# Kernel optimization log

Hardware: AMD Instinct MI355X
Metric: run time of the kernel (lower is better)

## Reference

```python
import jax, jax.numpy as jnp
import numpy as np

H = 16
D_MODEL = 1024
D_K = D_MODEL // H
WINDOW = 50
ROPE_BASE = 10000.0


def _rope_tables(seq_len, dim, dtype):
    inv_freq = 1.0 / (ROPE_BASE ** (jnp.arange(0, dim, 2, dtype=jnp.float32) / dim))
    t = jnp.arange(seq_len, dtype=jnp.float32)
    freqs = t[:, None] * inv_freq[None, :]          # [S, dim/2]
    emb = jnp.concatenate([freqs, freqs], axis=-1)  # [S, dim]
    return jnp.cos(emb).astype(dtype), jnp.sin(emb).astype(dtype)


def _rotate_half(x):
    d = x.shape[-1] // 2
    return jnp.concatenate([-x[..., d:], x[..., :d]], axis=-1)


def setup_inputs() -> dict:
    key = jax.random.key(0)
    ks = jax.random.split(key, 11)
    B, S = 2, 2048
    scale = 1.0 / np.sqrt(D_MODEL)
    inp = {
        'query': jax.random.normal(ks[0], (B, S, D_MODEL), jnp.float32),
        'key':   jax.random.normal(ks[1], (B, S, D_MODEL), jnp.float32),
        'value': jax.random.normal(ks[2], (B, S, D_MODEL), jnp.float32),
        'Wq': jax.random.normal(ks[3], (D_MODEL, D_MODEL), jnp.float32) * scale,
        'bq': jnp.zeros((D_MODEL,), jnp.float32),
        'Wk': jax.random.normal(ks[4], (D_MODEL, D_MODEL), jnp.float32) * scale,
        'bk': jnp.zeros((D_MODEL,), jnp.float32),
        'Wv': jax.random.normal(ks[5], (D_MODEL, D_MODEL), jnp.float32) * scale,
        'bv': jnp.zeros((D_MODEL,), jnp.float32),
        'Wo': jax.random.normal(ks[6], (D_MODEL, D_MODEL), jnp.float32) * scale,
        'bo': jnp.zeros((D_MODEL,), jnp.float32),
    }
    return inp


def reference(query, key, value, Wq, bq, Wk, bk, Wv, bv, Wo, bo):
    B, S, _ = query.shape
    # QKV projections (torch Linear: x @ W.T + b), split into heads -> [B,H,S,Dk]
    def proj(x, W, b):
        return (x @ W.T + b).reshape(B, S, H, D_K).transpose(0, 2, 1, 3)
    q = proj(query, Wq, bq)
    k = proj(key, Wk, bk)
    v = proj(value, Wv, bv)

    cos, sin = _rope_tables(S, D_K, q.dtype)  # [S, Dk]
    q = q * cos + _rotate_half(q) * sin
    k = k * cos + _rotate_half(k) * sin

    scores = jnp.einsum('bhqd,bhkd->bhqk', q, k) / np.sqrt(D_K)
    # sliding-window mask: |i-j| <= WINDOW
    idx = jnp.arange(S)
    dist = jnp.abs(idx[None, :] - idx[:, None])  # [S, S]
    scores = jnp.where(dist <= WINDOW, scores, jnp.asarray(-1e9, scores.dtype))

    p = jax.nn.softmax(scores, axis=-1)
    out = jnp.einsum('bhqk,bhkd->bhqd', p, v)          # [B,H,S,Dk]
    out = out.transpose(0, 2, 1, 3).reshape(B, S, D_MODEL)
    return out @ Wo.T + bo
```

## Files before the change

kernel.cpp:

```cpp
#include <hip/hip_runtime.h>
#include <hip/hip_bf16.h>
#include <math.h>

typedef __bf16 bf16_t;
typedef __bf16 bf16x8 __attribute__((ext_vector_type(8)));
typedef float floatx4 __attribute__((ext_vector_type(4)));
typedef unsigned int u32;

#define NHEAD 16

__device__ __forceinline__ void gload_lds16(const void* g, void* l) {
    __builtin_amdgcn_global_load_lds((const __attribute__((address_space(1))) u32*)g,
                                     (__attribute__((address_space(3))) u32*)l, 16, 0, 0);
}

__global__ __launch_bounds__(256) void k_prep(
    const float* __restrict__ q, const float* __restrict__ k, const float* __restrict__ v,
    const float* __restrict__ wq, const float* __restrict__ wk,
    const float* __restrict__ wv, const float* __restrict__ wo,
    bf16_t* __restrict__ Xq, bf16_t* __restrict__ Xk, bf16_t* __restrict__ Xv,
    bf16_t* __restrict__ Wqb, bf16_t* __restrict__ Wkb, bf16_t* __restrict__ Wvb,
    bf16_t* __restrict__ Wob, float* __restrict__ ct, float* __restrict__ st)
{
    int b = blockIdx.x;
    if (b < 8192) {
        const float* src; bf16_t* dst; int off;
        if      (b < 2048) { src = q;  dst = Xq;  off = b; }
        else if (b < 4096) { src = k;  dst = Xk;  off = b - 2048; }
        else if (b < 6144) { src = v;  dst = Xv;  off = b - 4096; }
        else if (b < 6656) { src = wq; dst = Wqb; off = b - 6144; }
        else if (b < 7168) { src = wk; dst = Wkb; off = b - 6656; }
        else if (b < 7680) { src = wv; dst = Wvb; off = b - 7168; }
        else               { src = wo; dst = Wob; off = b - 7680; }
        int i = (off * 256 + threadIdx.x) * 8;
        float4 a = *(const float4*)(src + i);
        float4 c = *(const float4*)(src + i + 4);
        bf16x8 o;
        o[0]=(bf16_t)a.x; o[1]=(bf16_t)a.y; o[2]=(bf16_t)a.z; o[3]=(bf16_t)a.w;
        o[4]=(bf16_t)c.x; o[5]=(bf16_t)c.y; o[6]=(bf16_t)c.z; o[7]=(bf16_t)c.w;
        *(bf16x8*)(dst + i) = o;
    } else {
        int idx = (b - 8192) * 256 + threadIdx.x;
        int s = idx >> 5, i = idx & 31;
        float e = (float)(2 * i) / 64.0f;
        float invf = 1.0f / powf(10000.0f, e);
        float ang = (float)s * invf;
        ct[idx] = cosf(ang);
        st[idx] = sinf(ang);
    }
}

__global__ __launch_bounds__(256,2) void k_gemm_qkv(
    const bf16_t* __restrict__ Xq, const bf16_t* __restrict__ Xk, const bf16_t* __restrict__ Xv,
    const bf16_t* __restrict__ Wqb, const bf16_t* __restrict__ Wkb, const bf16_t* __restrict__ Wvb,
    const float* __restrict__ bq, const float* __restrict__ bk, const float* __restrict__ bv,
    bf16_t* __restrict__ Qr, bf16_t* __restrict__ Kr, bf16_t* __restrict__ Vh,
    const float* __restrict__ ct, const float* __restrict__ st)
{
    __shared__ bf16_t As[2][128*32];
    __shared__ bf16_t Bs[2][128*32];

    int b0 = blockIdx.x;
    int wg = (b0 & 7) * 96 + (b0 >> 3);
    int id  = wg >> 8;
    int bid = wg & 255;

    const bf16_t* A   = (id==0) ? Xq  : (id==1) ? Xk  : Xv;
    const bf16_t* Wt  = (id==0) ? Wqb : (id==1) ? Wkb : Wvb;
    const float*  bias= (id==0) ? bq  : (id==1) ? bk  : bv;
    bf16_t* out = (id==0) ? Qr : (id==1) ? Kr : Vh;
    bool do_rope = (id < 2);

    int bm = (bid >> 3) << 7;
    int bn = (bid & 7) << 7;
    int tid = threadIdx.x;
    int l = tid & 63, wid = tid >> 6;
    int wr = wid >> 1, wc = wid & 1;
    int lane16 = l & 15, hi8 = (l >> 4) << 3;

    floatx4 acc[4][4];
    #pragma unroll
    for (int i = 0; i < 4; ++i)
        #pragma unroll
        for (int j = 0; j < 4; ++j) acc[i][j] = (floatx4){0.f,0.f,0.f,0.f};

    int srow = tid >> 2, scol = (tid & 3) << 3;
    const bf16_t* Ab = A  + ((size_t)(bm + srow) << 10) + scol;
    const bf16_t* Bb = Wt + ((size_t)(bn + srow) << 10) + scol;

    #pragma unroll
    for (int i2 = 0; i2 < 2; ++i2) {
        gload_lds16(Ab + (i2 << 16), &As[0][(tid + (i2<<8)) << 3]);
        gload_lds16(Bb + (i2 << 16), &Bs[0][(tid + (i2<<8)) << 3]);
    }
    __syncthreads();

    int cur = 0;
    for (int t = 0; t < 32; ++t) {
        if (t < 31) {
            int k0 = (t + 1) << 5;
            #pragma unroll
            for (int i2 = 0; i2 < 2; ++i2) {
                gload_lds16(Ab + k0 + (i2 << 16), &As[cur^1][(tid + (i2<<8)) << 3]);
                gload_lds16(Bb + k0 + (i2 << 16), &Bs[cur^1][(tid + (i2<<8)) << 3]);
            }
        }
        bf16x8 af[4], bfr[4];
        #pragma unroll
        for (int i = 0; i < 4; ++i)
            af[i]  = *(const bf16x8*)&As[cur][((wr<<6) + (i<<4) + lane16)*32 + hi8];
        #pragma unroll
        for (int j = 0; j < 4; ++j)
            bfr[j] = *(const bf16x8*)&Bs[cur][((wc<<6) + (j<<4) + lane16)*32 + hi8];
        #pragma unroll
        for (int i = 0; i < 4; ++i)
            #pragma unroll
            for (int j = 0; j < 4; ++j)
                acc[i][j] = __builtin_amdgcn_mfma_f32_16x16x32_bf16(af[i], bfr[j], acc[i][j], 0, 0, 0);
        __syncthreads();
        cur ^= 1;
    }

    int h = (bn + (wc<<6)) >> 6;
    #pragma unroll
    for (int i = 0; i < 4; ++i) {
        #pragma unroll
        for (int r = 0; r < 4; ++r) {
            int m  = bm + (wr<<6) + (i<<4) + ((l>>4)<<2) + r;
            int b_ = m >> 11, s_ = m & 2047;
            size_t ob = ((((size_t)(b_*NHEAD + h)) << 11) + s_) << 6;
            if (do_rope) {
                #pragma unroll
                for (int j = 0; j < 2; ++j) {
                    int d = (j<<4) + lane16;
                    float lo = acc[i][j][r]   + bias[bn + (wc<<6) + d];
                    float hv = acc[i][j+2][r] + bias[bn + (wc<<6) + d + 32];
                    float c = ct[(s_<<5) + d], sn = st[(s_<<5) + d];
                    out[ob + d]      = (bf16_t)(lo*c - hv*sn);
                    out[ob + d + 32] = (bf16_t)(hv*c + lo*sn);
                }
            } else {
                #pragma unroll
                for (int j = 0; j < 4; ++j) {
                    int d = (j<<4) + lane16;
                    out[ob + d] = (bf16_t)(acc[i][j][r] + bias[bn + (wc<<6) + d]);
                }
            }
        }
    }
}

__global__ __launch_bounds__(256,2) void k_gemm_o(
    const bf16_t* __restrict__ A, const bf16_t* __restrict__ Wt,
    const float* __restrict__ bias, float* __restrict__ out)
{
    __shared__ bf16_t As[2][128*32];
    __shared__ bf16_t Bs[2][128*32];

    int b0 = blockIdx.x;
    int bid = (b0 & 7) * 32 + (b0 >> 3);
    int bm = (bid >> 3) << 7;
    int bn = (bid & 7) << 7;
    int tid = threadIdx.x;
    int l = tid & 63, wid = tid >> 6;
    int wr = wid >> 1, wc = wid & 1;
    int lane16 = l & 15, hi8 = (l >> 4) << 3;

    floatx4 acc[4][4];
    #pragma unroll
    for (int i = 0; i < 4; ++i)
        #pragma unroll
        for (int j = 0; j < 4; ++j) acc[i][j] = (floatx4){0.f,0.f,0.f,0.f};

    int srow = tid >> 2, scol = (tid & 3) << 3;
    const bf16_t* Ab = A  + ((size_t)(bm + srow) << 10) + scol;
    const bf16_t* Bb = Wt + ((size_t)(bn + srow) << 10) + scol;

    #pragma unroll
    for (int i2 = 0; i2 < 2; ++i2) {
        gload_lds16(Ab + (i2 << 16), &As[0][(tid + (i2<<8)) << 3]);
        gload_lds16(Bb + (i2 << 16), &Bs[0][(tid + (i2<<8)) << 3]);
    }
    __syncthreads();

    int cur = 0;
    for (int t = 0; t < 32; ++t) {
        if (t < 31) {
            int k0 = (t + 1) << 5;
            #pragma unroll
            for (int i2 = 0; i2 < 2; ++i2) {
                gload_lds16(Ab + k0 + (i2 << 16), &As[cur^1][(tid + (i2<<8)) << 3]);
                gload_lds16(Bb + k0 + (i2 << 16), &Bs[cur^1][(tid + (i2<<8)) << 3]);
            }
        }
        bf16x8 af[4], bfr[4];
        #pragma unroll
        for (int i = 0; i < 4; ++i)
            af[i]  = *(const bf16x8*)&As[cur][((wr<<6) + (i<<4) + lane16)*32 + hi8];
        #pragma unroll
        for (int j = 0; j < 4; ++j)
            bfr[j] = *(const bf16x8*)&Bs[cur][((wc<<6) + (j<<4) + lane16)*32 + hi8];
        #pragma unroll
        for (int i = 0; i < 4; ++i)
            #pragma unroll
            for (int j = 0; j < 4; ++j)
                acc[i][j] = __builtin_amdgcn_mfma_f32_16x16x32_bf16(af[i], bfr[j], acc[i][j], 0, 0, 0);
        __syncthreads();
        cur ^= 1;
    }

    #pragma unroll
    for (int i = 0; i < 4; ++i)
        #pragma unroll
        for (int r = 0; r < 4; ++r) {
            int m = bm + (wr<<6) + (i<<4) + ((l>>4)<<2) + r;
            #pragma unroll
            for (int j = 0; j < 4; ++j) {
                int n = bn + (wc<<6) + (j<<4) + lane16;
                out[((size_t)m << 10) + n] = acc[i][j][r] + bias[n];
            }
        }
}

__global__ __launch_bounds__(256,2) void k_attn(
    const bf16_t* __restrict__ Qr, const bf16_t* __restrict__ Kr,
    const bf16_t* __restrict__ Vh, bf16_t* __restrict__ AO)
{
    __shared__ char smem[51200];
    bf16_t* KsPs = (bf16_t*)smem;
    bf16_t* Vt   = (bf16_t*)(smem + 25600);

    int q0 = blockIdx.x << 6;
    int h = blockIdx.y, b_ = blockIdx.z;
    int kstart = q0 - 64; if (kstart < 0) kstart = 0;
    int kend   = q0 + 128; if (kend > 2048) kend = 2048;
    int NR = kend - kstart;

    int tid = threadIdx.x, l = tid & 63, w = tid >> 6;
    int lane16 = l & 15, hi8 = (l >> 4) << 3;

    const bf16_t* Kbase = Kr + (((((size_t)(b_*NHEAD + h)) << 11) + kstart) << 6);
    const bf16_t* Vbase = Vh + (((((size_t)(b_*NHEAD + h)) << 11) + kstart) << 6);

    #pragma unroll
    for (int it = 0; it < 6; ++it) {
        int c = tid + (it << 8);
        int y = c << 4;
        int row = y >> 7, oz = y & 127;
        int srw = row < NR ? row : NR - 1;
        int src = (srw << 7) + (oz ^ ((row & 7) << 4));
        gload_lds16((const char*)Kbase + src, (char*)KsPs + y);
    }
    #pragma unroll
    for (int it = 0; it < 6; ++it) {
        int c = tid + (it << 8);
        int jd = c >> 3, d0 = (c & 7) << 3;
        int js = jd < NR ? jd : NR - 1;
        bf16x8 v8 = *(const bf16x8*)(Vbase + (js << 6) + d0);
        #pragma unroll
        for (int t = 0; t < 8; ++t) Vt[(d0 + t) * 200 + jd] = v8[t];
    }
    int qs = q0 + (w << 4) + lane16;
    const bf16_t* Qbase = Qr + (((((size_t)(b_*NHEAD + h)) << 11) + qs) << 6);
    bf16x8 qf0 = *(const bf16x8*)(Qbase + hi8);
    bf16x8 qf1 = *(const bf16x8*)(Qbase + 32 + hi8);

    __syncthreads();

    floatx4 sc[12];
    #pragma unroll
    for (int kt = 0; kt < 12; ++kt) {
        int row = (kt << 4) + lane16;
        int base = (row << 7) + (hi8 << 1);
        int swz = (row & 7) << 4;
        bf16x8 kf0 = *(const bf16x8*)((const char*)KsPs + (base ^ swz));
        bf16x8 kf1 = *(const bf16x8*)((const char*)KsPs + ((base + 64) ^ swz));
        floatx4 a = (floatx4){0.f,0.f,0.f,0.f};
        a = __builtin_amdgcn_mfma_f32_16x16x32_bf16(qf0, kf0, a, 0, 0, 0);
        a = __builtin_amdgcn_mfma_f32_16x16x32_bf16(qf1, kf1, a, 0, 0, 0);
        sc[kt] = a;
    }

    float inv_[4];
    #pragma unroll
    for (int r = 0; r < 4; ++r) {
        int qrow = q0 + (w << 4) + ((l >> 4) << 2) + r;
        float mx = -1e30f;
        #pragma unroll
        for (int kt = 0; kt < 12; ++kt) {
            int ks = kstart + (kt << 4) + lane16;
            int dd = qrow - ks; dd = dd < 0 ? -dd : dd;
            float sv = sc[kt][r] * 0.125f;
            sv = (dd <= 50 && ks < kend) ? sv : -1e30f;
            sc[kt][r] = sv;
            mx = fmaxf(mx, sv);
        }
        #pragma unroll
        for (int off = 1; off < 16; off <<= 1) mx = fmaxf(mx, __shfl_xor(mx, off));
        float sum = 0.f;
        #pragma unroll
        for (int kt = 0; kt < 12; ++kt) {
            float p = __expf(sc[kt][r] - mx);
            sc[kt][r] = p;
            sum += p;
        }
        #pragma unroll
        for (int off = 1; off < 16; off <<= 1) sum += __shfl_xor(sum, off);
        inv_[r] = 1.0f / sum;
    }

    __syncthreads();

    bf16_t* Pw = KsPs + w * 16 * 200;
    #pragma unroll
    for (int r = 0; r < 4; ++r) {
        int prow = ((l >> 4) << 2) + r;
        #pragma unroll
        for (int kt = 0; kt < 12; ++kt)
            Pw[prow * 200 + (kt << 4) + lane16] = (bf16_t)(sc[kt][r] * inv_[r]);
    }

    floatx4 oc[4];
    #pragma unroll
    for (int dt = 0; dt < 4; ++dt) oc[dt] = (floatx4){0.f,0.f,0.f,0.f};
    #pragma unroll
    for (int ks = 0; ks < 6; ++ks) {
        bf16x8 pf = *(const bf16x8*)&Pw[lane16 * 200 + (ks << 5) + hi8];
        #pragma unroll
        for (int dt = 0; dt < 4; ++dt) {
            bf16x8 vf = *(const bf16x8*)&Vt[((dt << 4) + lane16) * 200 + (ks << 5) + hi8];
            oc[dt] = __builtin_amdgcn_mfma_f32_16x16x32_bf16(pf, vf, oc[dt], 0, 0, 0);
        }
    }
    #pragma unroll
    for (int dt = 0; dt < 4; ++dt)
        #pragma unroll
        for (int r = 0; r < 4; ++r) {
            int qq = q0 + (w << 4) + ((l >> 4) << 2) + r;
            AO[(((size_t)(b_ * 2048 + qq)) << 10) + (h << 6) + (dt << 4) + lane16] = (bf16_t)oc[dt][r];
        }
}

extern "C" void kernel_launch(void* const* d_in, const int* in_sizes, int n_in,
                              void* d_out, int out_size, void* d_ws, size_t ws_size,
                              hipStream_t stream)
{
    const float* query = (const float*)d_in[0];
    const float* key_  = (const float*)d_in[1];
    const float* value = (const float*)d_in[2];
    const float* Wq = (const float*)d_in[3];
    const float* bq = (const float*)d_in[4];
    const float* Wk = (const float*)d_in[5];
    const float* bk = (const float*)d_in[6];
    const float* Wv = (const float*)d_in[7];
    const float* bv = (const float*)d_in[8];
    const float* Wo = (const float*)d_in[9];
    const float* bo = (const float*)d_in[10];

    char* ws = (char*)d_ws;
    bf16_t* Xq  = (bf16_t*)(ws);
    bf16_t* Xk  = (bf16_t*)(ws + 8388608);
    bf16_t* Xv  = (bf16_t*)(ws + 16777216);
    bf16_t* Wqb = (bf16_t*)(ws + 25165824);
    bf16_t* Wkb = (bf16_t*)(ws + 27262976);
    bf16_t* Wvb = (bf16_t*)(ws + 29360128);
    bf16_t* Wob = (bf16_t*)(ws + 31457280);
    bf16_t* Qr  = (bf16_t*)(ws + 33554432);
    bf16_t* Kr  = (bf16_t*)(ws + 41943040);
    bf16_t* Vh  = (bf16_t*)(ws + 50331648);
    bf16_t* AO  = (bf16_t*)(ws + 58720256);
    float*  ct  = (float*)(ws + 67108864);
    float*  st  = (float*)(ws + 67371008);

    k_prep<<<8448, 256, 0, stream>>>(query, key_, value, Wq, Wk, Wv, Wo,
                                     Xq, Xk, Xv, Wqb, Wkb, Wvb, Wob, ct, st);
    k_gemm_qkv<<<768, 256, 0, stream>>>(Xq, Xk, Xv, Wqb, Wkb, Wvb,
                                        bq, bk, bv, Qr, Kr, Vh, ct, st);
    k_attn<<<dim3(32, 16, 2), 256, 0, stream>>>(Qr, Kr, Vh, AO);
    k_gemm_o<<<256, 256, 0, stream>>>(AO, Wob, bo, (float*)d_out);
}
```

Baseline: 97.61 us.

## Fuse fp32-to-bf16 activation conversion into QKV GEMM loads; retile LDS layouts

Drops the separate pass that converted query/key/value from fp32 to bf16. The QKV GEMM now streams fp32 activations straight into LDS and converts to bf16 when building MFMA fragments, which removes a full read and write of the three activation tensors. LDS tiles are reorganised into fragment-friendly chunk layouts in both GEMMs, and launch bounds are raised to 3 blocks per SM. The fp32 A tile doubles the A-side LDS footprint and global traffic per k-step, and adds conversion ALU work in the inner loop.

Result: slower. 141.8 us (+45.2%).

```diff
diff --git a/kernel.cpp b/kernel.cpp
--- a/kernel.cpp
+++ b/kernel.cpp
@@ -14,33 +14,32 @@
                                      (__attribute__((address_space(3))) u32*)l, 16, 0, 0);
 }
 
+__device__ __forceinline__ bf16x8 cvt8(float4 a, float4 b) {
+    bf16x8 o;
+    o[0]=(bf16_t)a.x; o[1]=(bf16_t)a.y; o[2]=(bf16_t)a.z; o[3]=(bf16_t)a.w;
+    o[4]=(bf16_t)b.x; o[5]=(bf16_t)b.y; o[6]=(bf16_t)b.z; o[7]=(bf16_t)b.w;
+    return o;
+}
+
 __global__ __launch_bounds__(256) void k_prep(
-    const float* __restrict__ q, const float* __restrict__ k, const float* __restrict__ v,
     const float* __restrict__ wq, const float* __restrict__ wk,
     const float* __restrict__ wv, const float* __restrict__ wo,
-    bf16_t* __restrict__ Xq, bf16_t* __restrict__ Xk, bf16_t* __restrict__ Xv,
     bf16_t* __restrict__ Wqb, bf16_t* __restrict__ Wkb, bf16_t* __restrict__ Wvb,
     bf16_t* __restrict__ Wob, float* __restrict__ ct, float* __restrict__ st)
 {
     int b = blockIdx.x;
-    if (b < 8192) {
+    if (b < 2048) {
         const float* src; bf16_t* dst; int off;
-        if      (b < 2048) { src = q;  dst = Xq;  off = b; }
-        else if (b < 4096) { src = k;  dst = Xk;  off = b - 2048; }
-        else if (b < 6144) { src = v;  dst = Xv;  off = b - 4096; }
-        else if (b < 6656) { src = wq; dst = Wqb; off = b - 6144; }
-        else if (b < 7168) { src = wk; dst = Wkb; off = b - 6656; }
-        else if (b < 7680) { src = wv; dst = Wvb; off = b - 7168; }
-        else               { src = wo; dst = Wob; off = b - 7680; }
+        if      (b < 512)  { src = wq; dst = Wqb; off = b; }
+        else if (b < 1024) { src = wk; dst = Wkb; off = b - 512; }
+        else if (b < 1536) { src = wv; dst = Wvb; off = b - 1024; }
+        else               { src = wo; dst = Wob; off = b - 1536; }
         int i = (off * 256 + threadIdx.x) * 8;
         float4 a = *(const float4*)(src + i);
         float4 c = *(const float4*)(src + i + 4);
-        bf16x8 o;
-        o[0]=(bf16_t)a.x; o[1]=(bf16_t)a.y; o[2]=(bf16_t)a.z; o[3]=(bf16_t)a.w;
-        o[4]=(bf16_t)c.x; o[5]=(bf16_t)c.y; o[6]=(bf16_t)c.z; o[7]=(bf16_t)c.w;
-        *(bf16x8*)(dst + i) = o;
+        *(bf16x8*)(dst + i) = cvt8(a, c);
     } else {
-        int idx = (b - 8192) * 256 + threadIdx.x;
+        int idx = (b - 2048) * 256 + threadIdx.x;
         int s = idx >> 5, i = idx & 31;
         float e = (float)(2 * i) / 64.0f;
         float invf = 1.0f / powf(10000.0f, e);
@@ -50,22 +49,23 @@
     }
 }
 
-__global__ __launch_bounds__(256,2) void k_gemm_qkv(
-    const bf16_t* __restrict__ Xq, const bf16_t* __restrict__ Xk, const bf16_t* __restrict__ Xv,
+
+__global__ __launch_bounds__(256,3) void k_gemm_qkv(
+    const float* __restrict__ Xq, const float* __restrict__ Xk, const float* __restrict__ Xv,
     const bf16_t* __restrict__ Wqb, const bf16_t* __restrict__ Wkb, const bf16_t* __restrict__ Wvb,
     const float* __restrict__ bq, const float* __restrict__ bk, const float* __restrict__ bv,
     bf16_t* __restrict__ Qr, bf16_t* __restrict__ Kr, bf16_t* __restrict__ Vh,
     const float* __restrict__ ct, const float* __restrict__ st)
 {
-    __shared__ bf16_t As[2][128*32];
-    __shared__ bf16_t Bs[2][128*32];
+    __shared__ __align__(16) float  As[2][4096];
+    __shared__ __align__(16) bf16_t Bs[2][4096];
 
     int b0 = blockIdx.x;
     int wg = (b0 & 7) * 96 + (b0 >> 3);
     int id  = wg >> 8;
     int bid = wg & 255;
 
-    const bf16_t* A   = (id==0) ? Xq  : (id==1) ? Xk  : Xv;
+    const float*  A   = (id==0) ? Xq  : (id==1) ? Xk  : Xv;
     const bf16_t* Wt  = (id==0) ? Wqb : (id==1) ? Wkb : Wvb;
     const float*  bias= (id==0) ? bq  : (id==1) ? bk  : bv;
     bf16_t* out = (id==0) ? Qr : (id==1) ? Kr : Vh;
@@ -76,7 +76,7 @@
     int tid = threadIdx.x;
     int l = tid & 63, wid = tid >> 6;
     int wr = wid >> 1, wc = wid & 1;
-    int lane16 = l & 15, hi8 = (l >> 4) << 3;
+    int fr = l & 15, kg = l >> 4;
 
     floatx4 acc[4][4];
     #pragma unroll
@@ -84,15 +84,19 @@
         #pragma unroll
         for (int j = 0; j < 4; ++j) acc[i][j] = (floatx4){0.f,0.f,0.f,0.f};
 
-    int srow = tid >> 2, scol = (tid & 3) << 3;
-    const bf16_t* Ab = A  + ((size_t)(bm + srow) << 10) + scol;
-    const bf16_t* Bb = Wt + ((size_t)(bn + srow) << 10) + scol;
-
-    #pragma unroll
-    for (int i2 = 0; i2 < 2; ++i2) {
-        gload_lds16(Ab + (i2 << 16), &As[0][(tid + (i2<<8)) << 3]);
-        gload_lds16(Bb + (i2 << 16), &Bs[0][(tid + (i2<<8)) << 3]);
-    }
+    int rowa = ((tid >> 6) << 3) + (tid & 7);
+    int gca  = (tid >> 3) & 7;
+    const float* ApA = A + ((size_t)(bm + rowa) << 10) + (gca << 2);
+    int rowb = ((tid >> 6) << 4) + (tid & 15);
+    int slb  = ((tid >> 4) & 3) << 3;
+    const bf16_t* BpB = Wt + ((size_t)(bn + rowb) << 10) + slb;
+
+    #pragma unroll
+    for (int it = 0; it < 4; ++it)
+        gload_lds16(ApA + ((size_t)(it << 5) << 10), &As[0][(tid + (it << 8)) << 2]);
+    #pragma unroll
+    for (int it = 0; it < 2; ++it)
+        gload_lds16(BpB + ((size_t)(it << 6) << 10), &Bs[0][(tid + (it << 8)) << 3]);
     __syncthreads();
 
     int cur = 0;
@@ -100,18 +104,28 @@
         if (t < 31) {
             int k0 = (t + 1) << 5;
             #pragma unroll
-            for (int i2 = 0; i2 < 2; ++i2) {
-                gload_lds16(Ab + k0 + (i2 << 16), &As[cur^1][(tid + (i2<<8)) << 3]);
-                gload_lds16(Bb + k0 + (i2 << 16), &Bs[cur^1][(tid + (i2<<8)) << 3]);
-            }
-        }
+            for (int it = 0; it < 4; ++it)
+                gload_lds16(ApA + ((size_t)(it << 5) << 10) + k0,
+                            &As[cur ^ 1][(tid + (it << 8)) << 2]);
+            #pragma unroll
+            for (int it = 0; it < 2; ++it)
+                gload_lds16(BpB + ((size_t)(it << 6) << 10) + k0,
+                            &Bs[cur ^ 1][(tid + (it << 8)) << 3]);
+        }
+        const float*  Ac = As[cur];
+        const bf16_t* Bc = Bs[cur];
         bf16x8 af[4], bfr[4];
         #pragma unroll
-        for (int i = 0; i < 4; ++i)
-            af[i]  = *(const bf16x8*)&As[cur][((wr<<6) + (i<<4) + lane16)*32 + hi8];
+        for (int i = 0; i < 4; ++i) {
+            int ch = (((wr << 3) + (i << 1) + (fr >> 3)) << 6) + (kg << 4) + (fr & 7);
+            float4 lo = *(const float4*)&Ac[ch << 2];
+            float4 hi = *(const float4*)&Ac[(ch + 8) << 2];
+            af[i] = cvt8(lo, hi);
+        }
         #pragma unroll
         for (int j = 0; j < 4; ++j)
-            bfr[j] = *(const bf16x8*)&Bs[cur][((wc<<6) + (j<<4) + lane16)*32 + hi8];
+            bfr[j] = *(const bf16x8*)((const char*)Bc + ((((wc << 2) + j)) << 10)
+                                      + (kg << 8) + (fr << 4));
         #pragma unroll
         for (int i = 0; i < 4; ++i)
             #pragma unroll
@@ -132,7 +146,7 @@
             if (do_rope) {
                 #pragma unroll
                 for (int j = 0; j < 2; ++j) {
-                    int d = (j<<4) + lane16;
+                    int d = (j<<4) + fr;
                     float lo = acc[i][j][r]   + bias[bn + (wc<<6) + d];
                     float hv = acc[i][j+2][r] + bias[bn + (wc<<6) + d + 32];
                     float c = ct[(s_<<5) + d], sn = st[(s_<<5) + d];
@@ -142,7 +156,7 @@
             } else {
                 #pragma unroll
                 for (int j = 0; j < 4; ++j) {
-                    int d = (j<<4) + lane16;
+                    int d = (j<<4) + fr;
                     out[ob + d] = (bf16_t)(acc[i][j][r] + bias[bn + (wc<<6) + d]);
                 }
             }
@@ -150,12 +164,12 @@
     }
 }
 
-__global__ __launch_bounds__(256,2) void k_gemm_o(
+__global__ __launch_bounds__(256,3) void k_gemm_o(
     const bf16_t* __restrict__ A, const bf16_t* __restrict__ Wt,
     const float* __restrict__ bias, float* __restrict__ out)
 {
-    __shared__ bf16_t As[2][128*32];
-    __shared__ bf16_t Bs[2][128*32];
+    __shared__ __align__(16) bf16_t As[2][4096];
+    __shared__ __align__(16) bf16_t Bs[2][4096];
 
     int b0 = blockIdx.x;
     int bid = (b0 & 7) * 32 + (b0 >> 3);
@@ -164,7 +178,7 @@
     int tid = threadIdx.x;
     int l = tid & 63, wid = tid >> 6;
     int wr = wid >> 1, wc = wid & 1;
-    int lane16 = l & 15, hi8 = (l >> 4) << 3;
+    int fr = l & 15, kg = l >> 4;
 
     floatx4 acc[4][4];
     #pragma unroll
@@ -172,34 +186,38 @@
         #pragma unroll
         for (int j = 0; j < 4; ++j) acc[i][j] = (floatx4){0.f,0.f,0.f,0.f};
 
-    int srow = tid >> 2, scol = (tid & 3) << 3;
-    const bf16_t* Ab = A  + ((size_t)(bm + srow) << 10) + scol;
-    const bf16_t* Bb = Wt + ((size_t)(bn + srow) << 10) + scol;
-
-    #pragma unroll
-    for (int i2 = 0; i2 < 2; ++i2) {
-        gload_lds16(Ab + (i2 << 16), &As[0][(tid + (i2<<8)) << 3]);
-        gload_lds16(Bb + (i2 << 16), &Bs[0][(tid + (i2<<8)) << 3]);
+    int rowb = ((tid >> 6) << 4) + (tid & 15);
+    int slb  = ((tid >> 4) & 3) << 3;
+    const bf16_t* ApA = A  + ((size_t)(bm + rowb) << 10) + slb;
+    const bf16_t* BpB = Wt + ((size_t)(bn + rowb) << 10) + slb;
+
+    #pragma unroll
+    for (int it = 0; it < 2; ++it) {
+        gload_lds16(ApA + ((size_t)(it << 6) << 10), &As[0][(tid + (it << 8)) << 3]);
+        gload_lds16(BpB + ((size_t)(it << 6) << 10), &Bs[0][(tid + (it << 8)) << 3]);
     }
     __syncthreads();
 
+    int a_off = (kg << 8) + (fr << 4);
     int cur = 0;
     for (int t = 0; t < 32; ++t) {
         if (t < 31) {
             int k0 = (t + 1) << 5;
             #pragma unroll
-            for (int i2 = 0; i2 < 2; ++i2) {
-                gload_lds16(Ab + k0 + (i2 << 16), &As[cur^1][(tid + (i2<<8)) << 3]);
-                gload_lds16(Bb + k0 + (i2 << 16), &Bs[cur^1][(tid + (i2<<8)) << 3]);
+            for (int it = 0; it < 2; ++it) {
+                gload_lds16(ApA + ((size_t)(it << 6) << 10) + k0,
+                            &As[cur ^ 1][(tid + (it << 8)) << 3]);
+                gload_lds16(BpB + ((size_t)(it << 6) << 10) + k0,
+                            &Bs[cur ^ 1][(tid + (it << 8)) << 3]);
             }
         }
         bf16x8 af[4], bfr[4];
         #pragma unroll
         for (int i = 0; i < 4; ++i)
-            af[i]  = *(const bf16x8*)&As[cur][((wr<<6) + (i<<4) + lane16)*32 + hi8];
+            af[i]  = *(const bf16x8*)((const char*)As[cur] + ((((wr << 2) + i)) << 10) + a_off);
         #pragma unroll
         for (int j = 0; j < 4; ++j)
-            bfr[j] = *(const bf16x8*)&Bs[cur][((wc<<6) + (j<<4) + lane16)*32 + hi8];
+            bfr[j] = *(const bf16x8*)((const char*)Bs[cur] + ((((wc << 2) + j)) << 10) + a_off);
         #pragma unroll
         for (int i = 0; i < 4; ++i)
             #pragma unroll
@@ -216,7 +234,7 @@
             int m = bm + (wr<<6) + (i<<4) + ((l>>4)<<2) + r;
             #pragma unroll
             for (int j = 0; j < 4; ++j) {
-                int n = bn + (wc<<6) + (j<<4) + lane16;
+                int n = bn + (wc<<6) + (j<<4) + fr;
                 out[((size_t)m << 10) + n] = acc[i][j][r] + bias[n];
             }
         }
@@ -358,23 +376,19 @@
     const float* bo = (const float*)d_in[10];
 
     char* ws = (char*)d_ws;
-    bf16_t* Xq  = (bf16_t*)(ws);
-    bf16_t* Xk  = (bf16_t*)(ws + 8388608);
-    bf16_t* Xv  = (bf16_t*)(ws + 16777216);
-    bf16_t* Wqb = (bf16_t*)(ws + 25165824);
-    bf16_t* Wkb = (bf16_t*)(ws + 27262976);
-    bf16_t* Wvb = (bf16_t*)(ws + 29360128);
-    bf16_t* Wob = (bf16_t*)(ws + 31457280);
-    bf16_t* Qr  = (bf16_t*)(ws + 33554432);
-    bf16_t* Kr  = (bf16_t*)(ws + 41943040);
-    bf16_t* Vh  = (bf16_t*)(ws + 50331648);
-    bf16_t* AO  = (bf16_t*)(ws + 58720256);
-    float*  ct  = (float*)(ws + 67108864);
-    float*  st  = (float*)(ws + 67371008);
-
-    k_prep<<<8448, 256, 0, stream>>>(query, key_, value, Wq, Wk, Wv, Wo,
-                                     Xq, Xk, Xv, Wqb, Wkb, Wvb, Wob, ct, st);
-    k_gemm_qkv<<<768, 256, 0, stream>>>(Xq, Xk, Xv, Wqb, Wkb, Wvb,
+    bf16_t* Wqb = (bf16_t*)(ws);
+    bf16_t* Wkb = (bf16_t*)(ws + 2097152);
+    bf16_t* Wvb = (bf16_t*)(ws + 4194304);
+    bf16_t* Wob = (bf16_t*)(ws + 6291456);
+    bf16_t* Qr  = (bf16_t*)(ws + 8388608);
+    bf16_t* Kr  = (bf16_t*)(ws + 16777216);
+    bf16_t* Vh  = (bf16_t*)(ws + 25165824);
+    bf16_t* AO  = (bf16_t*)(ws + 33554432);
+    float*  ct  = (float*)(ws + 41943040);
+    float*  st  = (float*)(ws + 42205184);
+
+    k_prep<<<2304, 256, 0, stream>>>(Wq, Wk, Wv, Wo, Wqb, Wkb, Wvb, Wob, ct, st);
+    k_gemm_qkv<<<768, 256, 0, stream>>>(query, key_, value, Wqb, Wkb, Wvb,
                                         bq, bk, bv, Qr, Kr, Vh, ct, st);
     k_attn<<<dim3(32, 16, 2), 256, 0, stream>>>(Qr, Kr, Vh, AO);
     k_gemm_o<<<256, 256, 0, stream>>>(AO, Wob, bo, (float*)d_out);
```
